# Performance work log

Measured on AMD Instinct MI355X. Metric: run time of the kernel, lower is better.

Reference implementation:

```python
import jax, jax.numpy as jnp
import numpy as np

B, N, D = 8, 8192, 128   # D = in_dim + out_dim
H, KQ = 8, 64


def setup_inputs() -> dict:
    key = jax.random.key(0)
    k1, k2, k3, k4 = jax.random.split(key, 4)
    std = 0.02
    x = jax.random.normal(k1, (B, N, D), dtype=jnp.float32)
    # torch Linear weights are [out_features, in_features]
    Wk = jax.random.normal(k2, (H, KQ, D), dtype=jnp.float32) * std
    Wq = jax.random.normal(k3, (H, KQ, D), dtype=jnp.float32) * std
    Wv = jax.random.normal(k4, (H, D, D), dtype=jnp.float32) * std
    return {"x": x, "Wk": Wk, "Wq": Wq, "Wv": Wv}


def reference(x, Wk, Wq, Wv):
    # Per-head linear projections (Linear: y = x @ W^T), batched over heads.
    K = jnp.einsum('bnd,hkd->bhnk', x, Wk)   # [B,H,N,KQ]
    Q = jnp.einsum('bnd,hkd->bhnk', x, Wq)   # [B,H,N,KQ]
    V = jnp.einsum('bnd,hed->bhne', x, Wv)   # [B,H,N,D]
    # No softmax => (Q K^T) V == Q (K^T V): associative reorder avoids the
    # O(N^2) score matrix while computing identical math.
    KtV = jnp.einsum('bhnk,bhne->bhke', K, V)      # [B,H,KQ,D]
    out = jnp.einsum('bhnk,bhke->bne', Q, KtV)     # heads summed, [B,N,D]
    return out
```

## Files before the change

### kernel.cpp

```cpp
#include <hip/hip_runtime.h>
#include <hip/hip_bf16.h>

#define BB 8
#define NN 8192
#define DD 128
#define HH 8
#define KQ 64
#define SPLIT 32
#define NPB (NN / SPLIT)

typedef __attribute__((ext_vector_type(8))) short s16x8;
typedef __attribute__((ext_vector_type(4))) float f32x4;
typedef __attribute__((ext_vector_type(4))) unsigned short u16x4;
typedef __attribute__((ext_vector_type(8))) unsigned short u16x8;

__device__ __forceinline__ unsigned short bfr(float f) {
  unsigned u = __builtin_bit_cast(unsigned, f);
  u += 0x7fffu + ((u >> 16) & 1u);
  return (unsigned short)(u >> 16);
}

__global__ __launch_bounds__(256) void prep(
    const float* __restrict__ Wk, const float* __restrict__ Wq,
    const float* __restrict__ Wv, unsigned short* __restrict__ Wkbf,
    unsigned short* __restrict__ Wvbf, unsigned short* __restrict__ Wqt) {
  const int bx = blockIdx.x, t = threadIdx.x;
  if (bx < 64) {
    const int i = bx * 1024 + t * 4;
    float4 v = *(const float4*)(Wk + i);
    u16x4 o = {bfr(v.x), bfr(v.y), bfr(v.z), bfr(v.w)};
    *(u16x4*)(Wkbf + i) = o;
  } else if (bx < 192) {
    const int i = (bx - 64) * 1024 + t * 4;
    float4 v = *(const float4*)(Wv + i);
    u16x4 o = {bfr(v.x), bfr(v.y), bfr(v.z), bfr(v.w)};
    *(u16x4*)(Wvbf + i) = o;
  } else {
    const int h = bx - 192;
    const int d4 = (t & 31) * 4;
#pragma unroll
    for (int p = 0; p < 8; ++p) {
      const int k = (t >> 5) + p * 8;
      float4 v = *(const float4*)(Wq + (size_t)h * 8192 + k * DD + d4);
      unsigned short* dst = Wqt + (size_t)h * 8192;
      dst[(d4 + 0) * KQ + k] = bfr(v.x);
      dst[(d4 + 1) * KQ + k] = bfr(v.y);
      dst[(d4 + 2) * KQ + k] = bfr(v.z);
      dst[(d4 + 3) * KQ + k] = bfr(v.w);
    }
  }
}

__global__ __launch_bounds__(512) void gram_mfma(
    const float* __restrict__ x, float* __restrict__ part) {
  const int s = blockIdx.x, b = blockIdx.y;
  const int t = threadIdx.x, l = t & 63, w = t >> 6;
  __shared__ __align__(16) unsigned short xt[2][128 * 64];
  const float* xb = x + ((size_t)b * NN + (size_t)s * NPB) * DD;

  const int sd = t & 15;
  const int sn = (t >> 4) * 2;

  f32x4 acc[4][2];
#pragma unroll
  for (int i = 0; i < 4; ++i)
#pragma unroll
    for (int j = 0; j < 2; ++j) acc[i][j] = (f32x4){0.f, 0.f, 0.f, 0.f};

  float rv[8][2];
  auto load = [&](int sub) {
    const float* xs = xb + (size_t)sub * 64 * DD;
#pragma unroll
    for (int i = 0; i < 8; ++i)
#pragma unroll
      for (int j = 0; j < 2; ++j)
        rv[i][j] = xs[(size_t)(sn + j) * DD + sd + 16 * i];
  };
  auto stage = [&](int buf) {
    const int slot = sn >> 3;
#pragma unroll
    for (int i = 0; i < 8; ++i) {
      const int d = sd + 16 * i;
      unsigned v = (unsigned)bfr(rv[i][0]) | ((unsigned)bfr(rv[i][1]) << 16);
      char* dst = (char*)&xt[buf][0] + d * 128 +
                  (((slot ^ (d & 7)) << 4) | ((sn & 7) * 2));
      *(unsigned*)dst = v;
    }
  };

  load(0);
  stage(0);
  __syncthreads();

  const int d1s = (w & 1) * 64, d2s = (w >> 1) * 32;
  const int lr = l & 15, lk = l >> 4;
  const int nsub = NPB / 64;

  for (int sub = 0; sub < nsub; ++sub) {
    const int cur = sub & 1;
    if (sub + 1 < nsub) load(sub + 1);
#pragma unroll
    for (int kk = 0; kk < 2; ++kk) {
      s16x8 af[4], bv[2];
      const int kb = kk * 64 + lk * 16;
#pragma unroll
      for (int i = 0; i < 4; ++i) {
        const int row = d1s + i * 16 + lr;
        af[i] = *(const s16x8*)((const char*)&xt[cur][0] + row * 128 +
                                (kb ^ ((row & 7) << 4)));
      }
#pragma unroll
      for (int j = 0; j < 2; ++j) {
        const int row = d2s + j * 16 + lr;
        bv[j] = *(const s16x8*)((const char*)&xt[cur][0] + row * 128 +
                                (kb ^ ((row & 7) << 4)));
      }
#pragma unroll
      for (int i = 0; i < 4; ++i)
#pragma unroll
        for (int j = 0; j < 2; ++j)
          acc[i][j] =
              __builtin_amdgcn_mfma_f32_16x16x32_bf16(af[i], bv[j], acc[i][j], 0, 0, 0);
    }
    if (sub + 1 < nsub) stage(cur ^ 1);
    __syncthreads();
  }

  float* g = part + (((size_t)b * SPLIT + s) << 14);
#pragma unroll
  for (int i = 0; i < 4; ++i)
#pragma unroll
    for (int j = 0; j < 2; ++j)
#pragma unroll
      for (int r = 0; r < 4; ++r) {
        const int row = d1s + i * 16 + lk * 4 + r;
        const int col = d2s + j * 16 + lr;
        g[row * 128 + col] = acc[i][j][r];
      }
}

__global__ __launch_bounds__(256) void gram_reduce(
    const float* __restrict__ part, unsigned short* __restrict__ Gbf) {
  const int b = blockIdx.y;
  const int idx = blockIdx.x * 1024 + threadIdx.x * 4;
  const float* p = part + ((size_t)b * SPLIT << 14) + idx;
  float4 s = {0.f, 0.f, 0.f, 0.f};
  for (int i = 0; i < SPLIT; ++i) {
    float4 v = *(const float4*)(p + ((size_t)i << 14));
    s.x += v.x; s.y += v.y; s.z += v.z; s.w += v.w;
  }
  u16x4 o = {bfr(s.x), bfr(s.y), bfr(s.z), bfr(s.w)};
  *(u16x4*)(Gbf + ((size_t)b << 14) + idx) = o;
}

__global__ __launch_bounds__(256) void middle_fused(
    const unsigned short* __restrict__ Gbf, const unsigned short* __restrict__ Wkbf,
    const unsigned short* __restrict__ Wvbf, const unsigned short* __restrict__ Wqt,
    float* __restrict__ Mp) {
  const int b = blockIdx.x >> 3, h = blockIdx.x & 7;
  const int t = threadIdx.x, l = t & 63, w = t >> 6;
  const int lr = l & 15, lk = l >> 4;
  __shared__ __align__(16) unsigned short Gs[128 * 128];
  __shared__ __align__(16) unsigned short T1s[64 * 128];
  __shared__ __align__(16) unsigned short T2t[128 * 64];

  const unsigned short* gsrc = Gbf + ((size_t)b << 14);
#pragma unroll
  for (int c8 = 0; c8 < 8; ++c8) {
    const int c = t + c8 * 256;
    const int row = c >> 4, slot = c & 15;
    u16x8 v = *(const u16x8*)(gsrc + row * 128 + slot * 8);
    *(u16x8*)(&Gs[row * 128 + ((slot ^ (row & 15)) << 3)]) = v;
  }
  __syncthreads();

  const unsigned short* wk = Wkbf + ((size_t)h << 13);
  s16x8 aw[4];
#pragma unroll
  for (int ks = 0; ks < 4; ++ks)
    aw[ks] = *(const s16x8*)(wk + ((w * 16 + lr) << 7) + ks * 32 + lk * 8);
  f32x4 accA[8];
#pragma unroll
  for (int j = 0; j < 8; ++j) accA[j] = (f32x4){0.f, 0.f, 0.f, 0.f};
#pragma unroll
  for (int nj = 0; nj < 8; ++nj)
#pragma unroll
    for (int ks = 0; ks < 4; ++ks) {
      const int row = nj * 16 + lr;
      const int slot = (ks * 4 + lk) ^ (row & 15);
      s16x8 bfrag = *(const s16x8*)(&Gs[(row << 7) + (slot << 3)]);
      accA[nj] = __builtin_amdgcn_mfma_f32_16x16x32_bf16(aw[ks], bfrag, accA[nj], 0, 0, 0);
    }
#pragma unroll
  for (int nj = 0; nj < 8; ++nj)
#pragma unroll
    for (int r = 0; r < 4; ++r) {
      const int row = w * 16 + lk * 4 + r;
      const int col = nj * 16 + lr;
      const int slot = (col >> 3) ^ (row & 15);
      T1s[(row << 7) + (slot << 3) + (col & 7)] = bfr(accA[nj][r]);
    }
  __syncthreads();

  s16x8 a2[4];
#pragma unroll
  for (int ks = 0; ks < 4; ++ks) {
    const int row = w * 16 + lr;
    const int slot = (ks * 4 + lk) ^ (row & 15);
    a2[ks] = *(const s16x8*)(&T1s[(row << 7) + (slot << 3)]);
  }
  const unsigned short* wv = Wvbf + ((size_t)h << 14);
  f32x4 accB[8];
#pragma unroll
  for (int j = 0; j < 8; ++j) accB[j] = (f32x4){0.f, 0.f, 0.f, 0.f};
#pragma unroll
  for (int nj = 0; nj < 8; ++nj)
#pragma unroll
    for (int ks = 0; ks < 4; ++ks) {
      s16x8 bfrag = *(const s16x8*)(wv + (((size_t)(nj * 16 + lr)) << 7) + ks * 32 + lk * 8);
      accB[nj] = __builtin_amdgcn_mfma_f32_16x16x32_bf16(a2[ks], bfrag, accB[nj], 0, 0, 0);
    }
#pragma unroll
  for (int nj = 0; nj < 8; ++nj)
#pragma unroll
    for (int r = 0; r < 4; ++r) {
      const int e = nj * 16 + lr;
      const int k = w * 16 + lk * 4 + r;
      const int slot = (k >> 3) ^ (e & 7);
      T2t[(e << 6) + (slot << 3) + (k & 7)] = bfr(accB[nj][r]);
    }
  __syncthreads();

  const unsigned short* wq = Wqt + ((size_t)h << 13);
  float* mp = Mp + (((size_t)(b * 8 + h)) << 14);
#pragma unroll
  for (int p = 0; p < 2; ++p) {
    s16x8 a3[2];
#pragma unroll
    for (int ks = 0; ks < 2; ++ks) {
      const int row = (2 * w + p) * 16 + lr;
      const int slot = (ks * 4 + lk) ^ (row & 7);
      a3[ks] = *(const s16x8*)(&T2t[(row << 6) + (slot << 3)]);
    }
    f32x4 accC[8];
#pragma unroll
    for (int j = 0; j < 8; ++j) accC[j] = (f32x4){0.f, 0.f, 0.f, 0.f};
#pragma unroll
    for (int nj = 0; nj < 8; ++nj)
#pragma unroll
      for (int ks = 0; ks < 2; ++ks) {
        s16x8 bfrag = *(const s16x8*)(wq + ((nj * 16 + lr) << 6) + ks * 32 + lk * 8);
        accC[nj] = __builtin_amdgcn_mfma_f32_16x16x32_bf16(a3[ks], bfrag, accC[nj], 0, 0, 0);
      }
#pragma unroll
    for (int nj = 0; nj < 8; ++nj)
#pragma unroll
      for (int r = 0; r < 4; ++r) {
        const int row = (2 * w + p) * 16 + lk * 4 + r;
        const int col = nj * 16 + lr;
        mp[(row << 7) + col] = accC[nj][r];
      }
  }
}

__global__ __launch_bounds__(256) void m_reduce_t(
    const float* __restrict__ Mp, unsigned short* __restrict__ Mt) {
  const int b = blockIdx.y;
  const int idx = blockIdx.x * 1024 + threadIdx.x * 4;
  float4 s = {0.f, 0.f, 0.f, 0.f};
#pragma unroll
  for (int h = 0; h < 8; ++h) {
    float4 v = *(const float4*)(Mp + (((size_t)(b * 8 + h)) << 14) + idx);
    s.x += v.x; s.y += v.y; s.z += v.z; s.w += v.w;
  }
  u16x4 o = {bfr(s.x), bfr(s.y), bfr(s.z), bfr(s.w)};
  *(u16x4*)(Mt + ((size_t)b << 14) + idx) = o;
}

__global__ __launch_bounds__(256) void out_mfma(
    const float* __restrict__ x, const unsigned short* __restrict__ Mt,
    float* __restrict__ out) {
  const int b = blockIdx.y, t = threadIdx.x, l = t & 63, w = t >> 6;
  const int r0 = blockIdx.x * 128;
  __shared__ __align__(16) unsigned short mt[DD * DD];
  const unsigned short* msrc = Mt + (size_t)b * (DD * DD);
#pragma unroll
  for (int k = 0; k < 8; ++k) {
    const int c = t + k * 256;
    const int e = c >> 4, slot = c & 15;
    u16x8 v = *(const u16x8*)(msrc + e * DD + slot * 8);
    *(u16x8*)(&mt[e * DD + ((slot ^ (e & 15)) << 3)]) = v;
  }
  __syncthreads();

  const int rw = r0 + (w & 1) * 64, cw = (w >> 1) * 64;
  const int lr = l & 15, lk = l >> 4;
  f32x4 acc[4][4];
#pragma unroll
  for (int i = 0; i < 4; ++i)
#pragma unroll
    for (int j = 0; j < 4; ++j) acc[i][j] = (f32x4){0.f, 0.f, 0.f, 0.f};

  const float* xb = x + (size_t)b * NN * DD;
#pragma unroll
  for (int ks = 0; ks < 4; ++ks) {
    s16x8 af[4];
#pragma unroll
    for (int i = 0; i < 4; ++i) {
      const float* p = xb + (size_t)(rw + i * 16 + lr) * DD + ks * 32 + lk * 8;
      float4 v0 = *(const float4*)p;
      float4 v1 = *(const float4*)(p + 4);
      s16x8 a;
      a[0] = (short)bfr(v0.x); a[1] = (short)bfr(v0.y);
      a[2] = (short)bfr(v0.z); a[3] = (short)bfr(v0.w);
      a[4] = (short)bfr(v1.x); a[5] = (short)bfr(v1.y);
      a[6] = (short)bfr(v1.z); a[7] = (short)bfr(v1.w);
      af[i] = a;
    }
    s16x8 bv[4];
#pragma unroll
    for (int j = 0; j < 4; ++j) {
      const int e = cw + j * 16 + lr;
      const int slot = ks * 4 + lk;
      bv[j] = *(const s16x8*)(&mt[e * DD + ((slot ^ (e & 15)) << 3)]);
    }
#pragma unroll
    for (int i = 0; i < 4; ++i)
#pragma unroll
      for (int j = 0; j < 4; ++j)
        acc[i][j] =
            __builtin_amdgcn_mfma_f32_16x16x32_bf16(af[i], bv[j], acc[i][j], 0, 0, 0);
  }

  float* ob = out + (size_t)b * NN * DD;
#pragma unroll
  for (int i = 0; i < 4; ++i)
#pragma unroll
    for (int j = 0; j < 4; ++j)
#pragma unroll
      for (int r = 0; r < 4; ++r) {
        const int row = rw + i * 16 + lk * 4 + r;
        const int col = cw + j * 16 + lr;
        ob[(size_t)row * DD + col] = acc[i][j][r];
      }
}

extern "C" void kernel_launch(void* const* d_in, const int* in_sizes, int n_in,
                              void* d_out, int out_size, void* d_ws, size_t ws_size,
                              hipStream_t stream) {
  const float* x  = (const float*)d_in[0];
  const float* Wk = (const float*)d_in[1];
  const float* Wq = (const float*)d_in[2];
  const float* Wv = (const float*)d_in[3];
  float* out = (float*)d_out;
  float* ws  = (float*)d_ws;

  const size_t off_part = 0;
  const size_t off_Mp   = off_part + (size_t)BB * SPLIT * DD * DD;
  const size_t off_Gbf  = off_Mp + (size_t)BB * HH * DD * DD;
  const size_t off_Mt   = off_Gbf + (size_t)BB * DD * DD / 2;
  const size_t off_Wkbf = off_Mt + (size_t)BB * DD * DD / 2;
  const size_t off_Wvbf = off_Wkbf + (size_t)HH * KQ * DD / 2;
  const size_t off_Wqt  = off_Wvbf + (size_t)HH * DD * DD / 2;

  float* part = ws + off_part;
  float* Mp   = ws + off_Mp;
  unsigned short* Gbf  = (unsigned short*)(ws + off_Gbf);
  unsigned short* Mt   = (unsigned short*)(ws + off_Mt);
  unsigned short* Wkbf = (unsigned short*)(ws + off_Wkbf);
  unsigned short* Wvbf = (unsigned short*)(ws + off_Wvbf);
  unsigned short* Wqt  = (unsigned short*)(ws + off_Wqt);

  gram_mfma<<<dim3(SPLIT, BB), 512, 0, stream>>>(x, part);
  prep<<<200, 256, 0, stream>>>(Wk, Wq, Wv, Wkbf, Wvbf, Wqt);
  gram_reduce<<<dim3(16, BB), 256, 0, stream>>>(part, Gbf);
  middle_fused<<<64, 256, 0, stream>>>(Gbf, Wkbf, Wvbf, Wqt, Mp);
  m_reduce_t<<<dim3(16, BB), 256, 0, stream>>>(Mp, Mt);
  out_mfma<<<dim3(NN / 128, BB), 256, 0, stream>>>(x, Mt, out);
}
```

Baseline: 53.15 us.

## Fuse weight prep into gram kernel, store bf16 partials, shrink out tiles

Merges the weight-conversion kernel into the Gram kernel as four extra blocks, which removes one launch. Gram partial sums are now stored as bf16 instead of fp32, halving the traffic written and reread by the reduction. This adds rounding error, since each split's partial is rounded before summing. The output GEMM now uses 64-row tiles with one 16-row strip per wave, doubling the block count for better occupancy, at the cost of reloading the M tile into LDS more often.

Measured after the change: 73.36 us. +38.0%, slower.

```diff
diff --git a/kernel.cpp b/kernel.cpp
--- a/kernel.cpp
+++ b/kernel.cpp
@@ -19,42 +19,55 @@
   u += 0x7fffu + ((u >> 16) & 1u);
   return (unsigned short)(u >> 16);
 }
-
-__global__ __launch_bounds__(256) void prep(
-    const float* __restrict__ Wk, const float* __restrict__ Wq,
-    const float* __restrict__ Wv, unsigned short* __restrict__ Wkbf,
+__device__ __forceinline__ float b2f(unsigned short u) {
+  unsigned v = (unsigned)u << 16;
+  return __builtin_bit_cast(float, v);
+}
+
+__global__ __launch_bounds__(512) void gram_prep(
+    const float* __restrict__ x, const float* __restrict__ Wk,
+    const float* __restrict__ Wq, const float* __restrict__ Wv,
+    unsigned short* __restrict__ part, unsigned short* __restrict__ Wkbf,
     unsigned short* __restrict__ Wvbf, unsigned short* __restrict__ Wqt) {
   const int bx = blockIdx.x, t = threadIdx.x;
-  if (bx < 64) {
-    const int i = bx * 1024 + t * 4;
-    float4 v = *(const float4*)(Wk + i);
-    u16x4 o = {bfr(v.x), bfr(v.y), bfr(v.z), bfr(v.w)};
-    *(u16x4*)(Wkbf + i) = o;
-  } else if (bx < 192) {
-    const int i = (bx - 64) * 1024 + t * 4;
-    float4 v = *(const float4*)(Wv + i);
-    u16x4 o = {bfr(v.x), bfr(v.y), bfr(v.z), bfr(v.w)};
-    *(u16x4*)(Wvbf + i) = o;
-  } else {
-    const int h = bx - 192;
-    const int d4 = (t & 31) * 4;
-#pragma unroll
-    for (int p = 0; p < 8; ++p) {
-      const int k = (t >> 5) + p * 8;
-      float4 v = *(const float4*)(Wq + (size_t)h * 8192 + k * DD + d4);
-      unsigned short* dst = Wqt + (size_t)h * 8192;
-      dst[(d4 + 0) * KQ + k] = bfr(v.x);
-      dst[(d4 + 1) * KQ + k] = bfr(v.y);
-      dst[(d4 + 2) * KQ + k] = bfr(v.z);
-      dst[(d4 + 3) * KQ + k] = bfr(v.w);
-    }
-  }
-}
-
-__global__ __launch_bounds__(512) void gram_mfma(
-    const float* __restrict__ x, float* __restrict__ part) {
-  const int s = blockIdx.x, b = blockIdx.y;
-  const int t = threadIdx.x, l = t & 63, w = t >> 6;
+  if (bx < 4) {
+    if (bx == 0) {
+#pragma unroll 4
+      for (int it = 0; it < 32; ++it) {
+        const int i = it * 2048 + t * 4;
+        float4 v = *(const float4*)(Wk + i);
+        u16x4 o = {bfr(v.x), bfr(v.y), bfr(v.z), bfr(v.w)};
+        *(u16x4*)(Wkbf + i) = o;
+      }
+    } else if (bx <= 2) {
+      const int base = (bx - 1) * 65536;
+#pragma unroll 4
+      for (int it = 0; it < 32; ++it) {
+        const int i = base + it * 2048 + t * 4;
+        float4 v = *(const float4*)(Wv + i);
+        u16x4 o = {bfr(v.x), bfr(v.y), bfr(v.z), bfr(v.w)};
+        *(u16x4*)(Wvbf + i) = o;
+      }
+    } else {
+      const int d4 = (t & 31) * 4;
+#pragma unroll
+      for (int h = 0; h < 8; ++h)
+#pragma unroll
+        for (int p = 0; p < 4; ++p) {
+          const int k = (t >> 5) * 4 + p;
+          float4 v = *(const float4*)(Wq + (size_t)h * 8192 + k * DD + d4);
+          unsigned short* dst = Wqt + (size_t)h * 8192;
+          dst[(d4 + 0) * KQ + k] = bfr(v.x);
+          dst[(d4 + 1) * KQ + k] = bfr(v.y);
+          dst[(d4 + 2) * KQ + k] = bfr(v.z);
+          dst[(d4 + 3) * KQ + k] = bfr(v.w);
+        }
+    }
+    return;
+  }
+  const int g = bx - 4;
+  const int s = g & (SPLIT - 1), b = g >> 5;
+  const int l = t & 63, w = t >> 6;
   __shared__ __align__(16) unsigned short xt[2][128 * 64];
   const float* xb = x + ((size_t)b * NN + (size_t)s * NPB) * DD;
 
@@ -126,7 +139,7 @@
     __syncthreads();
   }
 
-  float* g = part + (((size_t)b * SPLIT + s) << 14);
+  unsigned short* gdst = part + (((size_t)b * SPLIT + s) << 14);
 #pragma unroll
   for (int i = 0; i < 4; ++i)
 #pragma unroll
@@ -135,21 +148,21 @@
       for (int r = 0; r < 4; ++r) {
         const int row = d1s + i * 16 + lk * 4 + r;
         const int col = d2s + j * 16 + lr;
-        g[row * 128 + col] = acc[i][j][r];
+        gdst[row * 128 + col] = bfr(acc[i][j][r]);
       }
 }
 
 __global__ __launch_bounds__(256) void gram_reduce(
-    const float* __restrict__ part, unsigned short* __restrict__ Gbf) {
+    const unsigned short* __restrict__ part, unsigned short* __restrict__ Gbf) {
   const int b = blockIdx.y;
   const int idx = blockIdx.x * 1024 + threadIdx.x * 4;
-  const float* p = part + ((size_t)b * SPLIT << 14) + idx;
-  float4 s = {0.f, 0.f, 0.f, 0.f};
+  const unsigned short* p = part + ((size_t)b * SPLIT << 14) + idx;
+  float s0 = 0.f, s1 = 0.f, s2 = 0.f, s3 = 0.f;
   for (int i = 0; i < SPLIT; ++i) {
-    float4 v = *(const float4*)(p + ((size_t)i << 14));
-    s.x += v.x; s.y += v.y; s.z += v.z; s.w += v.w;
-  }
-  u16x4 o = {bfr(s.x), bfr(s.y), bfr(s.z), bfr(s.w)};
+    u16x4 v = *(const u16x4*)(p + ((size_t)i << 14));
+    s0 += b2f(v[0]); s1 += b2f(v[1]); s2 += b2f(v[2]); s3 += b2f(v[3]);
+  }
+  u16x4 o = {bfr(s0), bfr(s1), bfr(s2), bfr(s3)};
   *(u16x4*)(Gbf + ((size_t)b << 14) + idx) = o;
 }
 
@@ -281,7 +294,7 @@
     const float* __restrict__ x, const unsigned short* __restrict__ Mt,
     float* __restrict__ out) {
   const int b = blockIdx.y, t = threadIdx.x, l = t & 63, w = t >> 6;
-  const int r0 = blockIdx.x * 128;
+  const int r0 = blockIdx.x * 64;
   __shared__ __align__(16) unsigned short mt[DD * DD];
   const unsigned short* msrc = Mt + (size_t)b * (DD * DD);
 #pragma unroll
@@ -293,56 +306,41 @@
   }
   __syncthreads();
 
-  const int rw = r0 + (w & 1) * 64, cw = (w >> 1) * 64;
   const int lr = l & 15, lk = l >> 4;
-  f32x4 acc[4][4];
-#pragma unroll
-  for (int i = 0; i < 4; ++i)
-#pragma unroll
-    for (int j = 0; j < 4; ++j) acc[i][j] = (f32x4){0.f, 0.f, 0.f, 0.f};
+  const int rw = r0 + w * 16;
+  f32x4 acc[8];
+#pragma unroll
+  for (int j = 0; j < 8; ++j) acc[j] = (f32x4){0.f, 0.f, 0.f, 0.f};
 
   const float* xb = x + (size_t)b * NN * DD;
 #pragma unroll
   for (int ks = 0; ks < 4; ++ks) {
-    s16x8 af[4];
-#pragma unroll
-    for (int i = 0; i < 4; ++i) {
-      const float* p = xb + (size_t)(rw + i * 16 + lr) * DD + ks * 32 + lk * 8;
-      float4 v0 = *(const float4*)p;
-      float4 v1 = *(const float4*)(p + 4);
-      s16x8 a;
-      a[0] = (short)bfr(v0.x); a[1] = (short)bfr(v0.y);
-      a[2] = (short)bfr(v0.z); a[3] = (short)bfr(v0.w);
-      a[4] = (short)bfr(v1.x); a[5] = (short)bfr(v1.y);
-      a[6] = (short)bfr(v1.z); a[7] = (short)bfr(v1.w);
-      af[i] = a;
-    }
-    s16x8 bv[4];
-#pragma unroll
-    for (int j = 0; j < 4; ++j) {
-      const int e = cw + j * 16 + lr;
-      const int slot = ks * 4 + lk;
-      bv[j] = *(const s16x8*)(&mt[e * DD + ((slot ^ (e & 15)) << 3)]);
-    }
-#pragma unroll
-    for (int i = 0; i < 4; ++i)
-#pragma unroll
-      for (int j = 0; j < 4; ++j)
-        acc[i][j] =
-            __builtin_amdgcn_mfma_f32_16x16x32_bf16(af[i], bv[j], acc[i][j], 0, 0, 0);
+    const float* p = xb + (size_t)(rw + lr) * DD + ks * 32 + lk * 8;
+    float4 v0 = *(const float4*)p;
+    float4 v1 = *(const float4*)(p + 4);
+    s16x8 af;
+    af[0] = (short)bfr(v0.x); af[1] = (short)bfr(v0.y);
+    af[2] = (short)bfr(v0.z); af[3] = (short)bfr(v0.w);
+    af[4] = (short)bfr(v1.x); af[5] = (short)bfr(v1.y);
+    af[6] = (short)bfr(v1.z); af[7] = (short)bfr(v1.w);
+    const int slot = ks * 4 + lk;
+#pragma unroll
+    for (int j = 0; j < 8; ++j) {
+      const int e = j * 16 + lr;
+      s16x8 bv = *(const s16x8*)(&mt[e * DD + ((slot ^ (e & 15)) << 3)]);
+      acc[j] = __builtin_amdgcn_mfma_f32_16x16x32_bf16(af, bv, acc[j], 0, 0, 0);
+    }
   }
 
   float* ob = out + (size_t)b * NN * DD;
 #pragma unroll
-  for (int i = 0; i < 4; ++i)
-#pragma unroll
-    for (int j = 0; j < 4; ++j)
-#pragma unroll
-      for (int r = 0; r < 4; ++r) {
-        const int row = rw + i * 16 + lk * 4 + r;
-        const int col = cw + j * 16 + lr;
-        ob[(size_t)row * DD + col] = acc[i][j][r];
-      }
+  for (int j = 0; j < 8; ++j)
+#pragma unroll
+    for (int r = 0; r < 4; ++r) {
+      const int row = rw + lk * 4 + r;
+      const int col = j * 16 + lr;
+      ob[(size_t)row * DD + col] = acc[j][r];
+    }
 }
 
 extern "C" void kernel_launch(void* const* d_in, const int* in_sizes, int n_in,
@@ -355,26 +353,25 @@
   float* out = (float*)d_out;
   float* ws  = (float*)d_ws;
 
-  const size_t off_part = 0;
-  const size_t off_Mp   = off_part + (size_t)BB * SPLIT * DD * DD;
-  const size_t off_Gbf  = off_Mp + (size_t)BB * HH * DD * DD;
+  const size_t off_Mp   = 0;
+  const size_t off_part = off_Mp + (size_t)BB * HH * DD * DD;
+  const size_t off_Gbf  = off_part + (size_t)BB * SPLIT * DD * DD / 2;
   const size_t off_Mt   = off_Gbf + (size_t)BB * DD * DD / 2;
   const size_t off_Wkbf = off_Mt + (size_t)BB * DD * DD / 2;
   const size_t off_Wvbf = off_Wkbf + (size_t)HH * KQ * DD / 2;
   const size_t off_Wqt  = off_Wvbf + (size_t)HH * DD * DD / 2;
 
-  float* part = ws + off_part;
   float* Mp   = ws + off_Mp;
+  unsigned short* part = (unsigned short*)(ws + off_part);
   unsigned short* Gbf  = (unsigned short*)(ws + off_Gbf);
   unsigned short* Mt   = (unsigned short*)(ws + off_Mt);
   unsigned short* Wkbf = (unsigned short*)(ws + off_Wkbf);
   unsigned short* Wvbf = (unsigned short*)(ws + off_Wvbf);
   unsigned short* Wqt  = (unsigned short*)(ws + off_Wqt);
 
-  gram_mfma<<<dim3(SPLIT, BB), 512, 0, stream>>>(x, part);
-  prep<<<200, 256, 0, stream>>>(Wk, Wq, Wv, Wkbf, Wvbf, Wqt);
+  gram_prep<<<4 + SPLIT * BB, 512, 0, stream>>>(x, Wk, Wq, Wv, part, Wkbf, Wvbf, Wqt);
   gram_reduce<<<dim3(16, BB), 256, 0, stream>>>(part, Gbf);
   middle_fused<<<64, 256, 0, stream>>>(Gbf, Wkbf, Wvbf, Wqt, Mp);
   m_reduce_t<<<dim3(16, BB), 256, 0, stream>>>(Mp, Mt);
-  out_mfma<<<dim3(NN / 128, BB), 256, 0, stream>>>(x, Mt, out);
-}
+  out_mfma<<<dim3(NN / 64, BB), 256, 0, stream>>>(x, Mt, out);
+}
```
